# Kernel tuning notes

Hardware: AMD Instinct MI355X
Metric: run time of the kernel (lower is better)

Reference implementation:

```python
import jax, jax.numpy as jnp
import numpy as np

N, E, D, H, B = 50000, 100000, 768, 1, 16
NEG_SLOPE = 0.2  # DGL EdgeGATConv default negative_slope


def setup_inputs() -> dict:
    key = jax.random.key(0)
    ks = jax.random.split(key, 16)
    s = 1.0 / np.sqrt(D)  # CaseGNN.reset_parameters: uniform(-1/sqrt(h_dim), 1/sqrt(h_dim))
    u = lambda k, shp: jax.random.uniform(k, shp, jnp.float32, -s, s)
    node_feats = jax.random.normal(ks[0], (N, D), jnp.float32)
    edge_feats = jax.random.normal(ks[1], (E, D), jnp.float32)
    src = jax.random.randint(ks[2], (E,), 0, N)
    # guarantee every node has >=1 incoming edge (DGL disallows zero in-degree)
    dst = jnp.concatenate([jnp.arange(N), jax.random.randint(ks[3], (E - N,), 0, N)])
    graph_offsets = jnp.arange(B, dtype=jnp.int32) * (N // B)  # first node of each batched graph
    return dict(
        node_feats=node_feats, edge_feats=edge_feats, src=src, dst=dst,
        graph_offsets=graph_offsets,
        W1=u(ks[4], (D, H * D)), We1=u(ks[5], (D, H * D)),
        al1=u(ks[6], (H, D)), ar1=u(ks[7], (H, D)), ae1=u(ks[8], (H, D)),
        b1=u(ks[9], (H * D,)),
        W2=u(ks[10], (D, H * D)), We2=u(ks[11], (D, H * D)),
        al2=u(ks[12], (H, D)), ar2=u(ks[13], (H, D)), ae2=u(ks[14], (H, D)),
        b2=u(ks[15], (H * D,)),
    )


def _edge_gat(x, ef, src, dst, W, We, al, ar, ae, b):
    """DGL EdgeGATConv (num_heads=H, residual=Identity since in==H*out, bias=True)."""
    n = x.shape[0]
    fs = (x @ W).reshape(n, H, -1)               # [N,H,Do] projected node feats
    fe = (ef @ We).reshape(ef.shape[0], H, -1)   # [E,H,Do] projected edge feats
    el = jnp.sum(fs * al, axis=-1)               # [N,H]
    er = jnp.sum(fs * ar, axis=-1)               # [N,H]
    ee = jnp.sum(fe * ae, axis=-1)               # [E,H]
    e = jax.nn.leaky_relu(el[src] + er[dst] + ee, NEG_SLOPE)  # [E,H]
    # edge_softmax over incoming edges of each dst node (numerically stable)
    emax = jax.ops.segment_max(e, dst, num_segments=n)
    emax = jnp.where(jnp.isfinite(emax), emax, 0.0)
    w = jnp.exp(e - emax[dst])
    wsum = jax.ops.segment_sum(w, dst, num_segments=n)[dst]
    a = w / jnp.where(wsum > 0, wsum, 1.0)       # [E,H]
    m = (fs[src] + fe) * a[..., None]            # [E,H,Do] messages
    rst = jax.ops.segment_sum(m, dst, num_segments=n)  # [N,H,Do]
    rst = rst + x.reshape(n, H, -1)              # identity residual
    rst = rst + b.reshape(1, H, -1)
    return rst.reshape(n, -1)                    # th.squeeze (H=1)


def reference(node_feats, edge_feats, src, dst, graph_offsets,
              W1, We1, al1, ar1, ae1, b1, W2, We2, al2, ar2, ae2, b2):
    h = _edge_gat(node_feats, edge_feats, src, dst, W1, We1, al1, ar1, ae1, b1)
    h = jax.nn.relu(h)  # dropouts are identity at eval
    h = _edge_gat(h, edge_feats, src, dst, W2, We2, al2, ar2, ae2, b2)
    return h[graph_offsets]  # first-node embedding of each graph, [B, D]
```

## Files before the change

### kernel.cpp

```cpp
#include <hip/hip_runtime.h>

#define D 768
#define CAP 64
#define MD1 16
#define NSLOTMAX 1040
#define VROWS 64
#define QCAP 64
#define NI 24
#define IC 32
#define NPROJ 768
#define NEG 0.2f

__device__ __forceinline__ float wave_reduce(float v) {
    #pragma unroll
    for (int o = 32; o > 0; o >>= 1) v += __shfl_down(v, o, 64);
    return v;
}

__device__ __forceinline__ float block_reduce_sum(float v, float* scratch) {
    int lane = threadIdx.x & 63;
    int wid  = threadIdx.x >> 6;
    v = wave_reduce(v);
    if (lane == 0) scratch[wid] = v;
    __syncthreads();
    if (threadIdx.x == 0) {
        float r = 0.f;
        #pragma unroll
        for (int w = 0; w < 4; ++w) r += scratch[w];
        scratch[0] = r;
    }
    __syncthreads();
    float r = scratch[0];
    __syncthreads();
    return r;
}

__global__ __launch_bounds__(256) void kA_proj_build(
        const float* W1, const float* We1, const float* W2, const float* We2,
        const float* al1, const float* ar1, const float* ae1,
        const float* al2, const float* ar2, const float* ae2,
        const int* __restrict__ dst, const int* __restrict__ goff,
        int E, int B, float* v, int* l2e, int* cnt) {
    int bid = blockIdx.x, tid = threadIdx.x;
    if (bid < NPROJ) {
        int task = bid * 4 + (tid >> 6);
        int lane = tid & 63;
        if (task >= 4 * D) return;
        int g = task / D, i = task % D;
        const float* W; const float* p1; const float* p2 = nullptr; int o1 = 0, o2 = 0;
        switch (g) {
            case 0: W = W1;  p1 = al1; p2 = ar1; o1 = 0;     o2 = D;     break;
            case 1: W = We1; p1 = ae1;           o1 = 2 * D;             break;
            case 2: W = W2;  p1 = al2; p2 = ar2; o1 = 3 * D; o2 = 4 * D; break;
            default:W = We2; p1 = ae2;           o1 = 5 * D;             break;
        }
        float s1 = 0.f, s2 = 0.f;
        for (int j = lane; j < D; j += 64) {
            float w = W[(long)i * D + j];
            s1 += w * p1[j];
            if (p2) s2 += w * p2[j];
        }
        #pragma unroll
        for (int o = 32; o > 0; o >>= 1) { s1 += __shfl_down(s1, o, 64); s2 += __shfl_down(s2, o, 64); }
        if (lane == 0) { v[o1 + i] = s1; if (p2) v[o2 + i] = s2; }
    } else {
        __shared__ int tg[16];
        int sb = bid - NPROJ, ns = gridDim.x - NPROJ;
        if (tid < B) tg[tid] = goff[tid];
        __syncthreads();
        for (int e = sb * 256 + tid; e < E; e += ns * 256) {
            int d = dst[e];
            for (int b = 0; b < B; ++b) {
                if (d == tg[b]) {
                    int pos = atomicAdd(&cnt[b], 1);
                    if (pos < CAP) l2e[b * CAP + pos] = e;
                }
            }
        }
    }
}

__global__ __launch_bounds__(256) void kB_match(
        const float* __restrict__ x, const float* __restrict__ ef,
        const int* __restrict__ src, const int* __restrict__ dst,
        const int* __restrict__ goff, const int* __restrict__ l2e,
        const int* __restrict__ cnt, const float* __restrict__ b1,
        const float* __restrict__ v, int E, int B, int nslot,
        int* mcnt, int* medge, int* msrc, float* melog, float* erj, float* h,
        int* vlg, int* vnp) {
    __shared__ int tnode[NSLOTMAX], tslot[NSLOTMAX];
    __shared__ int tn, qn;
    __shared__ int qe[QCAP], qs[QCAP], qsl[QCAP], qp[QCAP];
    int tid = threadIdx.x;
    if (tid == 0) { tn = 0; qn = 0; }
    __syncthreads();
    for (int s = tid; s < nslot; s += 256) {
        int node = -1; bool valid = false;
        if (s < B) { node = goff[s]; valid = true; }
        else { int rb = (s - B) >> 6, i = (s - B) & 63;
               int cb = cnt[rb]; if (cb > CAP) cb = CAP;
               if (i < cb) { node = src[l2e[rb * CAP + i]]; valid = true; } }
        if (valid) { int p = atomicAdd(&tn, 1); tnode[p] = node; tslot[p] = s; }
    }
    __syncthreads();
    int M = tn;
    const float* val1 = v;
    const float* var1 = v + D;
    const float* vae1 = v + 2 * D;
    int wv = tid >> 6, lane = tid & 63;
    {
        int s = blockIdx.x * 4 + wv;
        if (s < nslot) {
            int j = -1; bool valid = false;
            if (s < B) { j = goff[s]; valid = true; }
            else { int rb = (s - B) >> 6, i = (s - B) & 63;
                   int cb = cnt[rb]; if (cb > CAP) cb = CAP;
                   if (i < cb) { j = src[l2e[rb * CAP + i]]; valid = true; } }
            if (valid) {
                float acc = 0.f;
                for (int c = lane; c < D; c += 64) acc += x[(long)j * D + c] * var1[c];
                acc = wave_reduce(acc);
                if (lane == 0) erj[s] = acc;
                for (int c = lane; c < D; c += 64)
                    h[(long)s * D + c] = x[(long)j * D + c] + b1[c];
            }
        }
    }
    for (int e = blockIdx.x * 256 + tid; e < E; e += gridDim.x * 256) {
        int d = dst[e];
        for (int c = 0; c < M; ++c) {
            if (tnode[c] == d) {
                int sl = tslot[c];
                int p = atomicAdd(&mcnt[sl], 1);
                if (p < MD1) {
                    int sr = src[e];
                    medge[sl * MD1 + p] = e;
                    msrc[sl * MD1 + p] = sr;
                    int qq = atomicAdd(&qn, 1);
                    if (qq < QCAP) { qe[qq] = e; qs[qq] = sr; qsl[qq] = sl; qp[qq] = p; }
                    else {
                        float acc = 0.f;
                        for (int cc = 0; cc < D; ++cc)
                            acc += x[(long)sr * D + cc] * val1[cc] + ef[(long)e * D + cc] * vae1[cc];
                        melog[sl * MD1 + p] = acc;
                    }
                }
            }
        }
    }
    __syncthreads();
    int nq = qn; if (nq > QCAP) nq = QCAP;
    for (int m = wv; m < nq; m += 4) {
        int e = qe[m], sr = qs[m];
        float acc = 0.f;
        for (int c = lane; c < D; c += 64)
            acc += x[(long)sr * D + c] * val1[c] + ef[(long)e * D + c] * vae1[c];
        acc = wave_reduce(acc);
        if (lane == 0) melog[qsl[m] * MD1 + qp[m]] = acc;
    }
    if (blockIdx.x == 0 && tid < 64) {
        int base = 0;
        for (int s0 = 0; s0 < nslot; s0 += 64) {
            int s = s0 + tid;
            bool valid = false;
            if (s < B) valid = true;
            else if (s < nslot) {
                int rb = (s - B) >> 6, i = (s - B) & 63;
                int cb = cnt[rb]; if (cb > CAP) cb = CAP;
                valid = i < cb;
            }
            unsigned long long mb = __ballot(valid);
            if (valid) {
                int ci = base + __popcll(mb & ((1ULL << tid) - 1));
                if (ci < VROWS) vlg[ci] = s;
            }
            base += __popcll(mb);
        }
        if (tid == 0) *vnp = base < VROWS ? base : VROWS;
    }
}

__global__ __launch_bounds__(256) void kC_gemm1(
        const float* __restrict__ W1, const float* __restrict__ We1,
        const float* __restrict__ x, const float* __restrict__ ef,
        const int* __restrict__ mcnt, const int* __restrict__ medge,
        const int* __restrict__ msrc, const float* __restrict__ melog,
        const float* __restrict__ erj, const int* __restrict__ vlg,
        const int* __restrict__ vnp, float* h) {
    int tid = threadIdx.x;
    int q = blockIdx.x % 3, iy = (blockIdx.x / 3) % NI, rh = blockIdx.x / (3 * NI);
    int col = q * 256 + tid, i0 = iy * IC;
    __shared__ int vl_s[VROWS];
    __shared__ int vn_s, snm[32];
    __shared__ float smatt[32][MD1];
    __shared__ int ssrc[32][MD1], sedge[32][MD1];
    __shared__ float sgS[32][IC], sgE[32][IC];
    if (tid == 0) vn_s = *vnp;
    if (tid < VROWS) vl_s[tid] = vlg[tid];
    __syncthreads();
    int vn = vn_s;
    int half = (vn + 1) >> 1;
    int r0 = rh * half, r1 = r0 + half; if (r1 > vn) r1 = vn;
    int nr = r1 - r0;
    if (tid < nr) {
        int s = vl_s[r0 + tid];
        int nm = mcnt[s]; if (nm > MD1) nm = MD1;
        snm[tid] = nm;
        for (int k = 0; k < nm; ++k) {
            sedge[tid][k] = medge[s * MD1 + k];
            ssrc[tid][k]  = msrc[s * MD1 + k];
            smatt[tid][k] = melog[s * MD1 + k];
        }
        for (int a_ = 1; a_ < nm; ++a_) {
            int ke = sedge[tid][a_], ks = ssrc[tid][a_]; float kl = smatt[tid][a_];
            int b = a_ - 1;
            while (b >= 0 && sedge[tid][b] > ke) {
                sedge[tid][b+1] = sedge[tid][b]; ssrc[tid][b+1] = ssrc[tid][b];
                smatt[tid][b+1] = smatt[tid][b]; --b;
            }
            sedge[tid][b+1] = ke; ssrc[tid][b+1] = ks; smatt[tid][b+1] = kl;
        }
        float er = erj[s], mx = -1e30f;
        for (int k = 0; k < nm; ++k) {
            float l = smatt[tid][k] + er;
            l = l >= 0.f ? l : NEG * l;
            smatt[tid][k] = l; mx = fmaxf(mx, l);
        }
        float sum = 0.f;
        for (int k = 0; k < nm; ++k) { float p = expf(smatt[tid][k] - mx); smatt[tid][k] = p; sum += p; }
        float inv = 1.f / sum;
        for (int k = 0; k < nm; ++k) smatt[tid][k] *= inv;
    }
    __syncthreads();
    if (tid < 2 * nr) {
        int lr = tid >> 1, mat = tid & 1;
        int nm = snm[lr];
        float acc[IC];
        #pragma unroll
        for (int i = 0; i < IC; ++i) acc[i] = 0.f;
        if (mat == 0) {
            for (int k = 0; k < nm; ++k) {
                const float* p = x + (long)ssrc[lr][k] * D + i0;
                float w_ = smatt[lr][k];
                #pragma unroll
                for (int i = 0; i < IC; ++i) acc[i] += w_ * p[i];
            }
            #pragma unroll
            for (int i = 0; i < IC; ++i) sgS[lr][i] = acc[i];
        } else {
            for (int k = 0; k < nm; ++k) {
                const float* p = ef + (long)sedge[lr][k] * D + i0;
                float w_ = smatt[lr][k];
                #pragma unroll
                for (int i = 0; i < IC; ++i) acc[i] += w_ * p[i];
            }
            #pragma unroll
            for (int i = 0; i < IC; ++i) sgE[lr][i] = acc[i];
        }
    }
    __syncthreads();
    if (nr > 0) {
        float w[IC], we[IC];
        #pragma unroll
        for (int k = 0; k < IC; ++k) {
            w[k]  = W1[(long)(i0 + k) * D + col];
            we[k] = We1[(long)(i0 + k) * D + col];
        }
        for (int lr = 0; lr < nr; ++lr) {
            float acc = 0.f;
            #pragma unroll
            for (int k = 0; k < IC; ++k) acc += sgS[lr][k] * w[k] + sgE[lr][k] * we[k];
            atomicAdd(&h[(long)vl_s[r0 + lr] * D + col], acc);
        }
    }
}

__global__ __launch_bounds__(256) void kD_l2prep(
        const float* __restrict__ ef, const int* __restrict__ l2e,
        const int* __restrict__ cnt, const float* __restrict__ b2,
        const float* __restrict__ v, const float* __restrict__ h,
        float* elog2, float* er2, float* out, int B, int nslot) {
    int wv = threadIdx.x >> 6, lane = threadIdx.x & 63;
    int t = blockIdx.x * 4 + wv;
    const float* val2 = v + 3 * D;
    const float* var2 = v + 4 * D;
    const float* vae2 = v + 5 * D;
    if (t < B) {
        float acc = 0.f;
        for (int c = lane; c < D; c += 64) acc += fmaxf(h[(long)t * D + c], 0.f) * var2[c];
        acc = wave_reduce(acc);
        if (lane == 0) er2[t] = acc;
        for (int c = lane; c < D; c += 64)
            out[(long)t * D + c] = fmaxf(h[(long)t * D + c], 0.f) + b2[c];
    } else if (t < nslot) {
        int rb = (t - B) >> 6, i = (t - B) & 63;
        int cb = cnt[rb]; if (cb > CAP) cb = CAP;
        if (i < cb) {
            int e = l2e[rb * CAP + i];
            const float* hs = h + (long)t * D;
            float acc = 0.f;
            for (int c = lane; c < D; c += 64)
                acc += fmaxf(hs[c], 0.f) * val2[c] + ef[(long)e * D + c] * vae2[c];
            acc = wave_reduce(acc);
            if (lane == 0) elog2[rb * CAP + i] = acc;
        }
    }
}

__global__ __launch_bounds__(256) void kE_gemm2(
        const float* __restrict__ W2, const float* __restrict__ We2,
        const float* __restrict__ ef, const int* __restrict__ l2e,
        const int* __restrict__ cnt, const float* __restrict__ elog2,
        const float* __restrict__ er2, const float* __restrict__ h,
        float* out, int B) {
    __shared__ float smatt[16][CAP];
    __shared__ int sedge[16][CAP], spos[16][CAP], sdeg[16];
    __shared__ float sgS[16][IC], sgE[16][IC];
    int tid = threadIdx.x;
    int q = blockIdx.x % 3, iy = blockIdx.x / 3;
    int col = q * 256 + tid, i0 = iy * IC;
    if (tid < B) {
        int b = tid;
        int deg = cnt[b]; if (deg > CAP) deg = CAP;
        sdeg[b] = deg;
        for (int k = 0; k < deg; ++k) { sedge[b][k] = l2e[b * CAP + k]; spos[b][k] = k; }
        for (int a_ = 1; a_ < deg; ++a_) {
            int ke = sedge[b][a_], kp = spos[b][a_]; int c = a_ - 1;
            while (c >= 0 && sedge[b][c] > ke) {
                sedge[b][c+1] = sedge[b][c]; spos[b][c+1] = spos[b][c]; --c;
            }
            sedge[b][c+1] = ke; spos[b][c+1] = kp;
        }
        float er = er2[b], mx = -1e30f;
        for (int k = 0; k < deg; ++k) {
            float l = elog2[b * CAP + spos[b][k]] + er;
            l = l >= 0.f ? l : NEG * l;
            smatt[b][k] = l; mx = fmaxf(mx, l);
        }
        float sum = 0.f;
        for (int k = 0; k < deg; ++k) { float p = expf(smatt[b][k] - mx); smatt[b][k] = p; sum += p; }
        float inv = sum > 0.f ? 1.f / sum : 0.f;
        for (int k = 0; k < deg; ++k) smatt[b][k] *= inv;
    }
    __syncthreads();
    if (tid < 2 * B) {
        int r = tid >> 1, mat = tid & 1;
        int deg = sdeg[r];
        float acc[IC];
        #pragma unroll
        for (int i = 0; i < IC; ++i) acc[i] = 0.f;
        if (mat == 0) {
            for (int k = 0; k < deg; ++k) {
                const float* hs = h + (long)(B + r * CAP + spos[r][k]) * D + i0;
                float w_ = smatt[r][k];
                #pragma unroll
                for (int i = 0; i < IC; ++i) acc[i] += w_ * fmaxf(hs[i], 0.f);
            }
            #pragma unroll
            for (int i = 0; i < IC; ++i) sgS[r][i] = acc[i];
        } else {
            for (int k = 0; k < deg; ++k) {
                const float* p = ef + (long)sedge[r][k] * D + i0;
                float w_ = smatt[r][k];
                #pragma unroll
                for (int i = 0; i < IC; ++i) acc[i] += w_ * p[i];
            }
            #pragma unroll
            for (int i = 0; i < IC; ++i) sgE[r][i] = acc[i];
        }
    }
    __syncthreads();
    {
        float w[IC], we[IC];
        #pragma unroll
        for (int k = 0; k < IC; ++k) {
            w[k]  = W2[(long)(i0 + k) * D + col];
            we[k] = We2[(long)(i0 + k) * D + col];
        }
        for (int r = 0; r < B; ++r) {
            float acc = 0.f;
            #pragma unroll
            for (int k = 0; k < IC; ++k) acc += sgS[r][k] * w[k] + sgE[r][k] * we[k];
            atomicAdd(&out[(long)r * D + col], acc);
        }
    }
}

extern "C" void kernel_launch(void* const* d_in, const int* in_sizes, int n_in,
                              void* d_out, int out_size, void* d_ws, size_t ws_size,
                              hipStream_t stream) {
    const float* x    = (const float*)d_in[0];
    const float* ef   = (const float*)d_in[1];
    const int*   src  = (const int*)d_in[2];
    const int*   dst  = (const int*)d_in[3];
    const int*   goff = (const int*)d_in[4];
    const float* W1   = (const float*)d_in[5];
    const float* We1  = (const float*)d_in[6];
    const float* al1  = (const float*)d_in[7];
    const float* ar1  = (const float*)d_in[8];
    const float* ae1  = (const float*)d_in[9];
    const float* b1   = (const float*)d_in[10];
    const float* W2   = (const float*)d_in[11];
    const float* We2  = (const float*)d_in[12];
    const float* al2  = (const float*)d_in[13];
    const float* ar2  = (const float*)d_in[14];
    const float* ae2  = (const float*)d_in[15];
    const float* b2   = (const float*)d_in[16];
    float* out = (float*)d_out;

    int E = in_sizes[2];
    int B = in_sizes[4];
    int nslot = B + B * CAP;

    float* ws    = (float*)d_ws;
    float* v     = ws;
    int*   l2e   = (int*)(v + 6 * D);
    int*   cnt   = l2e + B * CAP;
    int*   mcnt  = cnt + B;
    int*   medge = mcnt + nslot;
    int*   msrc  = medge + nslot * MD1;
    float* melog = (float*)(msrc + nslot * MD1);
    float* erj   = melog + nslot * MD1;
    int*   vlg   = (int*)(erj + nslot);
    int*   vnp   = vlg + VROWS;
    float* elog2 = (float*)(vnp + 1);
    float* er2   = elog2 + B * CAP;
    float* h     = er2 + B;

    int egrid = (E + 255) / 256;

    hipMemsetAsync(cnt, 0, (size_t)(B + nslot) * sizeof(int), stream);
    hipLaunchKernelGGL(kA_proj_build, dim3(NPROJ + egrid), dim3(256), 0, stream,
                       W1, We1, W2, We2, al1, ar1, ae1, al2, ar2, ae2,
                       dst, goff, E, B, v, l2e, cnt);
    hipLaunchKernelGGL(kB_match, dim3(egrid), dim3(256), 0, stream,
                       x, ef, src, dst, goff, l2e, cnt, b1, v, E, B, nslot,
                       mcnt, medge, msrc, melog, erj, h, vlg, vnp);
    hipLaunchKernelGGL(kC_gemm1, dim3(3 * NI * 2), dim3(256), 0, stream,
                       W1, We1, x, ef, mcnt, medge, msrc, melog, erj, vlg, vnp, h);
    hipLaunchKernelGGL(kD_l2prep, dim3((nslot + 3) / 4), dim3(256), 0, stream,
                       ef, l2e, cnt, b2, v, h, elog2, er2, out, B, nslot);
    hipLaunchKernelGGL(kE_gemm2, dim3(3 * NI), dim3(256), 0, stream,
                       W2, We2, ef, l2e, cnt, elog2, er2, h, out, B);
}
```

Measured before the change: 72.95 us.

## Fuse attention-logit computation into GEMM kernels and drop the layer-2 prep kernel

Per-edge attention logits for layer 1 are no longer computed in the match kernel. Instead each gemm1 block recomputes them redundantly from x and ef, using chunked dot products accumulated into shared memory with atomics. The separate kD_l2prep kernel is removed: kE_gemm2 now computes the layer-2 logits, the er term and the residual+bias init itself, and out is zeroed inside kB_match. This removes one launch and the global round trip for the logits, but every block in the GEMM grids now repeats the same logit dot products, adding redundant memory reads.

```diff
diff --git a/kernel.cpp b/kernel.cpp
--- a/kernel.cpp
+++ b/kernel.cpp
@@ -5,7 +5,6 @@
 #define MD1 16
 #define NSLOTMAX 1040
 #define VROWS 64
-#define QCAP 64
 #define NI 24
 #define IC 32
 #define NPROJ 768
@@ -15,24 +14,6 @@
     #pragma unroll
     for (int o = 32; o > 0; o >>= 1) v += __shfl_down(v, o, 64);
     return v;
-}
-
-__device__ __forceinline__ float block_reduce_sum(float v, float* scratch) {
-    int lane = threadIdx.x & 63;
-    int wid  = threadIdx.x >> 6;
-    v = wave_reduce(v);
-    if (lane == 0) scratch[wid] = v;
-    __syncthreads();
-    if (threadIdx.x == 0) {
-        float r = 0.f;
-        #pragma unroll
-        for (int w = 0; w < 4; ++w) r += scratch[w];
-        scratch[0] = r;
-    }
-    __syncthreads();
-    float r = scratch[0];
-    __syncthreads();
-    return r;
 }
 
 __global__ __launch_bounds__(256) void kA_proj_build(
@@ -86,13 +67,12 @@
         const int* __restrict__ goff, const int* __restrict__ l2e,
         const int* __restrict__ cnt, const float* __restrict__ b1,
         const float* __restrict__ v, int E, int B, int nslot,
-        int* mcnt, int* medge, int* msrc, float* melog, float* erj, float* h,
-        int* vlg, int* vnp) {
+        int* mcnt, int* medge, int* msrc, float* erj, float* h,
+        int* vlg, int* vnp, float* out) {
     __shared__ int tnode[NSLOTMAX], tslot[NSLOTMAX];
-    __shared__ int tn, qn;
-    __shared__ int qe[QCAP], qs[QCAP], qsl[QCAP], qp[QCAP];
+    __shared__ int tn;
     int tid = threadIdx.x;
-    if (tid == 0) { tn = 0; qn = 0; }
+    if (tid == 0) tn = 0;
     __syncthreads();
     for (int s = tid; s < nslot; s += 256) {
         int node = -1; bool valid = false;
@@ -104,10 +84,9 @@
     }
     __syncthreads();
     int M = tn;
-    const float* val1 = v;
     const float* var1 = v + D;
-    const float* vae1 = v + 2 * D;
     int wv = tid >> 6, lane = tid & 63;
+    for (int i = blockIdx.x * 256 + tid; i < B * D; i += gridDim.x * 256) out[i] = 0.f;
     {
         int s = blockIdx.x * 4 + wv;
         if (s < nslot) {
@@ -133,30 +112,11 @@
                 int sl = tslot[c];
                 int p = atomicAdd(&mcnt[sl], 1);
                 if (p < MD1) {
-                    int sr = src[e];
                     medge[sl * MD1 + p] = e;
-                    msrc[sl * MD1 + p] = sr;
-                    int qq = atomicAdd(&qn, 1);
-                    if (qq < QCAP) { qe[qq] = e; qs[qq] = sr; qsl[qq] = sl; qp[qq] = p; }
-                    else {
-                        float acc = 0.f;
-                        for (int cc = 0; cc < D; ++cc)
-                            acc += x[(long)sr * D + cc] * val1[cc] + ef[(long)e * D + cc] * vae1[cc];
-                        melog[sl * MD1 + p] = acc;
-                    }
+                    msrc[sl * MD1 + p]  = src[e];
                 }
             }
         }
-    }
-    __syncthreads();
-    int nq = qn; if (nq > QCAP) nq = QCAP;
-    for (int m = wv; m < nq; m += 4) {
-        int e = qe[m], sr = qs[m];
-        float acc = 0.f;
-        for (int c = lane; c < D; c += 64)
-            acc += x[(long)sr * D + c] * val1[c] + ef[(long)e * D + c] * vae1[c];
-        acc = wave_reduce(acc);
-        if (lane == 0) melog[qsl[m] * MD1 + qp[m]] = acc;
     }
     if (blockIdx.x == 0 && tid < 64) {
         int base = 0;
@@ -184,19 +144,22 @@
         const float* __restrict__ W1, const float* __restrict__ We1,
         const float* __restrict__ x, const float* __restrict__ ef,
         const int* __restrict__ mcnt, const int* __restrict__ medge,
-        const int* __restrict__ msrc, const float* __restrict__ melog,
-        const float* __restrict__ erj, const int* __restrict__ vlg,
-        const int* __restrict__ vnp, float* h) {
+        const int* __restrict__ msrc, const float* __restrict__ erj,
+        const int* __restrict__ vlg, const int* __restrict__ vnp,
+        const float* __restrict__ v, float* h) {
     int tid = threadIdx.x;
     int q = blockIdx.x % 3, iy = (blockIdx.x / 3) % NI, rh = blockIdx.x / (3 * NI);
     int col = q * 256 + tid, i0 = iy * IC;
     __shared__ int vl_s[VROWS];
     __shared__ int vn_s, snm[32];
-    __shared__ float smatt[32][MD1];
+    __shared__ float slog[32][MD1];
     __shared__ int ssrc[32][MD1], sedge[32][MD1];
     __shared__ float sgS[32][IC], sgE[32][IC];
+    const float* val1 = v;
+    const float* vae1 = v + 2 * D;
     if (tid == 0) vn_s = *vnp;
     if (tid < VROWS) vl_s[tid] = vlg[tid];
+    for (int i = tid; i < 32 * MD1; i += 256) ((float*)slog)[i] = 0.f;
     __syncthreads();
     int vn = vn_s;
     int half = (vn + 1) >> 1;
@@ -209,27 +172,40 @@
         for (int k = 0; k < nm; ++k) {
             sedge[tid][k] = medge[s * MD1 + k];
             ssrc[tid][k]  = msrc[s * MD1 + k];
-            smatt[tid][k] = melog[s * MD1 + k];
         }
         for (int a_ = 1; a_ < nm; ++a_) {
-            int ke = sedge[tid][a_], ks = ssrc[tid][a_]; float kl = smatt[tid][a_];
+            int ke = sedge[tid][a_], ks = ssrc[tid][a_];
             int b = a_ - 1;
             while (b >= 0 && sedge[tid][b] > ke) {
-                sedge[tid][b+1] = sedge[tid][b]; ssrc[tid][b+1] = ssrc[tid][b];
-                smatt[tid][b+1] = smatt[tid][b]; --b;
-            }
-            sedge[tid][b+1] = ke; ssrc[tid][b+1] = ks; smatt[tid][b+1] = kl;
-        }
-        float er = erj[s], mx = -1e30f;
+                sedge[tid][b+1] = sedge[tid][b]; ssrc[tid][b+1] = ssrc[tid][b]; --b;
+            }
+            sedge[tid][b+1] = ke; ssrc[tid][b+1] = ks;
+        }
+    }
+    __syncthreads();
+    for (int t = tid; t < nr * MD1 * 6; t += 256) {
+        int lr = t / (MD1 * 6), rem = t % (MD1 * 6), k = rem / 6, ch = rem % 6;
+        if (k >= snm[lr]) continue;
+        int c0 = ch * 128;
+        const float* px = x + (long)ssrc[lr][k] * D + c0;
+        const float* pe = ef + (long)sedge[lr][k] * D + c0;
+        float acc = 0.f;
+        for (int c = 0; c < 128; ++c) acc += px[c] * val1[c0 + c] + pe[c] * vae1[c0 + c];
+        atomicAdd(&slog[lr][k], acc);
+    }
+    __syncthreads();
+    if (tid < nr) {
+        int nm = snm[tid];
+        float er = erj[vl_s[r0 + tid]], mx = -1e30f;
         for (int k = 0; k < nm; ++k) {
-            float l = smatt[tid][k] + er;
+            float l = slog[tid][k] + er;
             l = l >= 0.f ? l : NEG * l;
-            smatt[tid][k] = l; mx = fmaxf(mx, l);
+            slog[tid][k] = l; mx = fmaxf(mx, l);
         }
         float sum = 0.f;
-        for (int k = 0; k < nm; ++k) { float p = expf(smatt[tid][k] - mx); smatt[tid][k] = p; sum += p; }
-        float inv = 1.f / sum;
-        for (int k = 0; k < nm; ++k) smatt[tid][k] *= inv;
+        for (int k = 0; k < nm; ++k) { float p = expf(slog[tid][k] - mx); slog[tid][k] = p; sum += p; }
+        float inv = sum > 0.f ? 1.f / sum : 0.f;
+        for (int k = 0; k < nm; ++k) slog[tid][k] *= inv;
     }
     __syncthreads();
     if (tid < 2 * nr) {
@@ -241,7 +217,7 @@
         if (mat == 0) {
             for (int k = 0; k < nm; ++k) {
                 const float* p = x + (long)ssrc[lr][k] * D + i0;
-                float w_ = smatt[lr][k];
+                float w_ = slog[lr][k];
                 #pragma unroll
                 for (int i = 0; i < IC; ++i) acc[i] += w_ * p[i];
             }
@@ -250,7 +226,7 @@
         } else {
             for (int k = 0; k < nm; ++k) {
                 const float* p = ef + (long)sedge[lr][k] * D + i0;
-                float w_ = smatt[lr][k];
+                float w_ = slog[lr][k];
                 #pragma unroll
                 for (int i = 0; i < IC; ++i) acc[i] += w_ * p[i];
             }
@@ -275,50 +251,23 @@
     }
 }
 
-__global__ __launch_bounds__(256) void kD_l2prep(
+__global__ __launch_bounds__(256) void kE_gemm2(
+        const float* __restrict__ W2, const float* __restrict__ We2,
         const float* __restrict__ ef, const int* __restrict__ l2e,
         const int* __restrict__ cnt, const float* __restrict__ b2,
         const float* __restrict__ v, const float* __restrict__ h,
-        float* elog2, float* er2, float* out, int B, int nslot) {
-    int wv = threadIdx.x >> 6, lane = threadIdx.x & 63;
-    int t = blockIdx.x * 4 + wv;
-    const float* val2 = v + 3 * D;
-    const float* var2 = v + 4 * D;
-    const float* vae2 = v + 5 * D;
-    if (t < B) {
-        float acc = 0.f;
-        for (int c = lane; c < D; c += 64) acc += fmaxf(h[(long)t * D + c], 0.f) * var2[c];
-        acc = wave_reduce(acc);
-        if (lane == 0) er2[t] = acc;
-        for (int c = lane; c < D; c += 64)
-            out[(long)t * D + c] = fmaxf(h[(long)t * D + c], 0.f) + b2[c];
-    } else if (t < nslot) {
-        int rb = (t - B) >> 6, i = (t - B) & 63;
-        int cb = cnt[rb]; if (cb > CAP) cb = CAP;
-        if (i < cb) {
-            int e = l2e[rb * CAP + i];
-            const float* hs = h + (long)t * D;
-            float acc = 0.f;
-            for (int c = lane; c < D; c += 64)
-                acc += fmaxf(hs[c], 0.f) * val2[c] + ef[(long)e * D + c] * vae2[c];
-            acc = wave_reduce(acc);
-            if (lane == 0) elog2[rb * CAP + i] = acc;
-        }
-    }
-}
-
-__global__ __launch_bounds__(256) void kE_gemm2(
-        const float* __restrict__ W2, const float* __restrict__ We2,
-        const float* __restrict__ ef, const int* __restrict__ l2e,
-        const int* __restrict__ cnt, const float* __restrict__ elog2,
-        const float* __restrict__ er2, const float* __restrict__ h,
         float* out, int B) {
-    __shared__ float smatt[16][CAP];
+    __shared__ float slog[16][CAP], ser[16];
     __shared__ int sedge[16][CAP], spos[16][CAP], sdeg[16];
     __shared__ float sgS[16][IC], sgE[16][IC];
     int tid = threadIdx.x;
     int q = blockIdx.x % 3, iy = blockIdx.x / 3;
     int col = q * 256 + tid, i0 = iy * IC;
+    const float* val2 = v + 3 * D;
+    const float* var2 = v + 4 * D;
+    const float* vae2 = v + 5 * D;
+    for (int i = tid; i < 16 * CAP; i += 256) ((float*)slog)[i] = 0.f;
+    if (tid >= 16 * CAP / 256 * 0 && tid < 16) ser[tid] = 0.f;
     if (tid < B) {
         int b = tid;
         int deg = cnt[b]; if (deg > CAP) deg = CAP;
@@ -331,16 +280,39 @@
             }
             sedge[b][c+1] = ke; spos[b][c+1] = kp;
         }
-        float er = er2[b], mx = -1e30f;
+    }
+    __syncthreads();
+    for (int t = tid; t < B * 6; t += 256) {
+        int b = t / 6, ch = t % 6, c0 = ch * 128;
+        const float* hb = h + (long)b * D + c0;
+        float acc = 0.f;
+        for (int c = 0; c < 128; ++c) acc += fmaxf(hb[c], 0.f) * var2[c0 + c];
+        atomicAdd(&ser[b], acc);
+    }
+    for (int t = tid; t < B * CAP * 6; t += 256) {
+        int b = t / (CAP * 6), rem = t % (CAP * 6), k = rem / 6, ch = rem % 6;
+        if (k >= sdeg[b]) continue;
+        int c0 = ch * 128;
+        const float* hs = h + (long)(B + b * CAP + spos[b][k]) * D + c0;
+        const float* pe = ef + (long)sedge[b][k] * D + c0;
+        float acc = 0.f;
+        for (int c = 0; c < 128; ++c)
+            acc += fmaxf(hs[c], 0.f) * val2[c0 + c] + pe[c] * vae2[c0 + c];
+        atomicAdd(&slog[b][k], acc);
+    }
+    __syncthreads();
+    if (tid < B) {
+        int b = tid, deg = sdeg[b];
+        float er = ser[b], mx = -1e30f;
         for (int k = 0; k < deg; ++k) {
-            float l = elog2[b * CAP + spos[b][k]] + er;
+            float l = slog[b][k] + er;
             l = l >= 0.f ? l : NEG * l;
-            smatt[b][k] = l; mx = fmaxf(mx, l);
+            slog[b][k] = l; mx = fmaxf(mx, l);
         }
         float sum = 0.f;
-        for (int k = 0; k < deg; ++k) { float p = expf(smatt[b][k] - mx); smatt[b][k] = p; sum += p; }
+        for (int k = 0; k < deg; ++k) { float p = expf(slog[b][k] - mx); slog[b][k] = p; sum += p; }
         float inv = sum > 0.f ? 1.f / sum : 0.f;
-        for (int k = 0; k < deg; ++k) smatt[b][k] *= inv;
+        for (int k = 0; k < deg; ++k) slog[b][k] *= inv;
     }
     __syncthreads();
     if (tid < 2 * B) {
@@ -352,7 +324,7 @@
         if (mat == 0) {
             for (int k = 0; k < deg; ++k) {
                 const float* hs = h + (long)(B + r * CAP + spos[r][k]) * D + i0;
-                float w_ = smatt[r][k];
+                float w_ = slog[r][k];
                 #pragma unroll
                 for (int i = 0; i < IC; ++i) acc[i] += w_ * fmaxf(hs[i], 0.f);
             }
@@ -361,7 +333,7 @@
         } else {
             for (int k = 0; k < deg; ++k) {
                 const float* p = ef + (long)sedge[r][k] * D + i0;
-                float w_ = smatt[r][k];
+                float w_ = slog[r][k];
                 #pragma unroll
                 for (int i = 0; i < IC; ++i) acc[i] += w_ * p[i];
             }
@@ -378,7 +350,7 @@
             we[k] = We2[(long)(i0 + k) * D + col];
         }
         for (int r = 0; r < B; ++r) {
-            float acc = 0.f;
+            float acc = (iy == 0) ? fmaxf(h[(long)r * D + col], 0.f) + b2[col] : 0.f;
             #pragma unroll
             for (int k = 0; k < IC; ++k) acc += sgS[r][k] * w[k] + sgE[r][k] * we[k];
             atomicAdd(&out[(long)r * D + col], acc);
@@ -419,13 +391,10 @@
     int*   mcnt  = cnt + B;
     int*   medge = mcnt + nslot;
     int*   msrc  = medge + nslot * MD1;
-    float* melog = (float*)(msrc + nslot * MD1);
-    float* erj   = melog + nslot * MD1;
+    float* erj   = (float*)(msrc + nslot * MD1);
     int*   vlg   = (int*)(erj + nslot);
     int*   vnp   = vlg + VROWS;
-    float* elog2 = (float*)(vnp + 1);
-    float* er2   = elog2 + B * CAP;
-    float* h     = er2 + B;
+    float* h     = (float*)(vnp + 1);
 
     int egrid = (E + 255) / 256;
 
@@ -435,11 +404,9 @@
                        dst, goff, E, B, v, l2e, cnt);
     hipLaunchKernelGGL(kB_match, dim3(egrid), dim3(256), 0, stream,
                        x, ef, src, dst, goff, l2e, cnt, b1, v, E, B, nslot,
-                       mcnt, medge, msrc, melog, erj, h, vlg, vnp);
+                       mcnt, medge, msrc, erj, h, vlg, vnp, out);
     hipLaunchKernelGGL(kC_gemm1, dim3(3 * NI * 2), dim3(256), 0, stream,
-                       W1, We1, x, ef, mcnt, medge, msrc, melog, erj, vlg, vnp, h);
-    hipLaunchKernelGGL(kD_l2prep, dim3((nslot + 3) / 4), dim3(256), 0, stream,
-                       ef, l2e, cnt, b2, v, h, elog2, er2, out, B, nslot);
+                       W1, We1, x, ef, mcnt, medge, msrc, erj, vlg, vnp, v, h);
     hipLaunchKernelGGL(kE_gemm2, dim3(3 * NI), dim3(256), 0, stream,
-                       W2, We2, ef, l2e, cnt, elog2, er2, h, out, B);
-}
+                       W2, We2, ef, l2e, cnt, b2, v, h, out, B);
+}
```

After: 144.6 us. +98.2%, slower.
